# Optimization experiments

Measured on AMD Instinct MI355X. Metric: run time of the kernel, lower is better.

## Reference

```python
import jax, jax.numpy as jnp
import numpy as np

VOCAB = 50257
FEAT = 512
EPS = 1e-12  # F.normalize default eps


def setup_inputs() -> dict:
    key = jax.random.key(0)
    k1, k2, k3 = jax.random.split(key, 3)
    token_ids = jax.random.randint(k1, (32, 4096), 0, VOCAB)
    # nn.Linear(vocab, feat): weight [FEAT, VOCAB], bias [FEAT]
    W = jax.random.normal(k2, (FEAT, VOCAB), dtype=jnp.float32) * 0.02
    b = jax.random.normal(k3, (FEAT,), dtype=jnp.float32) * 0.02
    return {"token_ids": token_ids, "W": W, "b": b}


def reference(token_ids, W, b):
    # one_hot(ids) @ W.T + b  ==  gather rows of W.T at ids, then add bias
    feats = W.T[token_ids] + b  # [B, S, FEAT]
    norm = jnp.sqrt(jnp.sum(feats * feats, axis=-1, keepdims=True))
    return feats / jnp.maximum(norm, EPS)
```

## Files before the change

### kernel.cpp

```cpp
#include <hip/hip_runtime.h>
#include <hip/hip_bf16.h>

#define VOCAB 50257
#define FEAT 512
#define NTOK (32 * 4096)
#define EPS 1e-12f
#define NFT 8

typedef float f32x4 __attribute__((ext_vector_type(4)));

__device__ __forceinline__ unsigned short f2bf(float x) {
    __hip_bfloat16 h = __float2bfloat16(x);
    unsigned short u;
    __builtin_memcpy(&u, &h, 2);
    return u;
}
__device__ __forceinline__ float bfround(float x) {
    return __bfloat162float(__float2bfloat16(x));
}
__device__ __forceinline__ float bflo(unsigned int w) {
    unsigned int u = w << 16; float f; __builtin_memcpy(&f, &u, 4); return f;
}
__device__ __forceinline__ float bfhi(unsigned int w) {
    unsigned int u = w & 0xffff0000u; float f; __builtin_memcpy(&f, &u, 4); return f;
}

__global__ __launch_bounds__(256) void transpose_bias_bf16(
        const float* __restrict__ W, const float* __restrict__ b,
        unsigned short* __restrict__ Wt, float* __restrict__ partial) {
    __shared__ float tile[64][65];
    __shared__ float psum[4][64];
    const int t  = threadIdx.x;
    const int l  = t & 63;
    const int w  = t >> 6;
    const int v0 = blockIdx.x * 64;
    const int f0 = blockIdx.y * 64;
    const int c  = l & 15;
    const int r  = l >> 4;
    const int vb = v0 + c * 4;

    float p[4] = {0.f, 0.f, 0.f, 0.f};
#pragma unroll
    for (int k = 0; k < 4; ++k) {
        const int fl = w * 16 + k * 4 + r;
        const int f  = f0 + fl;
        f32x4 x;
        if (vb + 3 < VOCAB) {
            __builtin_memcpy(&x, W + (size_t)f * VOCAB + vb, 16);
        } else {
#pragma unroll
            for (int i = 0; i < 4; ++i)
                x[i] = (vb + i < VOCAB) ? W[(size_t)f * VOCAB + vb + i] : 0.0f;
        }
        const float bf = b[f];
#pragma unroll
        for (int i = 0; i < 4; ++i) {
            const float xi = x[i] + bf;
            tile[fl][c * 4 + i] = xi;
            const float xr = bfround(xi);
            p[i] += xr * xr;
        }
    }

#pragma unroll
    for (int i = 0; i < 4; ++i) {
        float s = p[i];
        s += __shfl_xor(s, 16, 64);
        s += __shfl_xor(s, 32, 64);
        if (r == 0) psum[w][c * 4 + i] = s;
    }
    __syncthreads();

    if (t < 64) {
        const int v = v0 + t;
        if (v < VOCAB)
            partial[blockIdx.y * VOCAB + v] =
                psum[0][t] + psum[1][t] + psum[2][t] + psum[3][t];
    }

#pragma unroll
    for (int ps = 0; ps < 2; ++ps) {
        const int idx = t + 256 * ps;
        const int vl  = idx >> 3;
        const int ch  = idx & 7;
        const int v   = v0 + vl;
        if (v < VOCAB) {
            unsigned int pk[4];
#pragma unroll
            for (int j = 0; j < 4; ++j) {
                const int f = ch * 8 + 2 * j;
                pk[j] = (unsigned int)f2bf(tile[f][vl]) |
                        ((unsigned int)f2bf(tile[f + 1][vl]) << 16);
            }
            *(uint4*)(Wt + (size_t)v * FEAT + f0 + ch * 8) =
                make_uint4(pk[0], pk[1], pk[2], pk[3]);
        }
    }
}

__global__ __launch_bounds__(256) void norm_table(const float* __restrict__ partial,
                                                  float* __restrict__ invn) {
    const int v = blockIdx.x * 256 + threadIdx.x;
    if (v >= VOCAB) return;
    float s = 0.0f;
#pragma unroll
    for (int j = 0; j < NFT; ++j) s += partial[j * VOCAB + v];
    invn[v] = 1.0f / fmaxf(sqrtf(s), EPS);
}

__global__ __launch_bounds__(256) void encode_bf16(
        const int* __restrict__ ids, const unsigned short* __restrict__ Wt,
        const float* __restrict__ invn, float* __restrict__ out) {
    const int tok  = (int)((blockIdx.x * (unsigned long long)blockDim.x + threadIdx.x) >> 6);
    const int lane = threadIdx.x & 63;
    if (tok >= NTOK) return;

    const int id = ids[tok];
    const uint4 rr = *(const uint4*)(Wt + (size_t)id * FEAT + lane * 8);
    const float inv = invn[id];

    float x[8];
    x[0] = bflo(rr.x); x[1] = bfhi(rr.x);
    x[2] = bflo(rr.y); x[3] = bfhi(rr.y);
    x[4] = bflo(rr.z); x[5] = bfhi(rr.z);
    x[6] = bflo(rr.w); x[7] = bfhi(rr.w);

    f32x4 o0 = {x[0] * inv, x[1] * inv, x[2] * inv, x[3] * inv};
    f32x4 o1 = {x[4] * inv, x[5] * inv, x[6] * inv, x[7] * inv};
    f32x4* dst = (f32x4*)(out + (size_t)tok * FEAT + lane * 8);
    __builtin_nontemporal_store(o0, dst);
    __builtin_nontemporal_store(o1, dst + 1);
}

__global__ __launch_bounds__(256) void encode_direct(const int* __restrict__ ids,
                                                     const float* __restrict__ W,
                                                     const float* __restrict__ bias,
                                                     float* __restrict__ out) {
    const int tok  = (int)((blockIdx.x * (unsigned long long)blockDim.x + threadIdx.x) >> 6);
    const int lane = threadIdx.x & 63;
    if (tok >= NTOK) return;

    const int id = ids[tok];
    float x[8];
    float s = 0.0f;
#pragma unroll
    for (int j = 0; j < 8; ++j) {
        const int f = lane * 8 + j;
        x[j] = W[(size_t)f * VOCAB + id] + bias[f];
        s += x[j] * x[j];
    }
#pragma unroll
    for (int off = 32; off > 0; off >>= 1)
        s += __shfl_xor(s, off, 64);

    const float inv = 1.0f / fmaxf(sqrtf(s), EPS);
    float4 o0 = make_float4(x[0] * inv, x[1] * inv, x[2] * inv, x[3] * inv);
    float4 o1 = make_float4(x[4] * inv, x[5] * inv, x[6] * inv, x[7] * inv);
    float4* dst = (float4*)(out + (size_t)tok * FEAT + lane * 8);
    dst[0] = o0;
    dst[1] = o1;
}

extern "C" void kernel_launch(void* const* d_in, const int* in_sizes, int n_in,
                              void* d_out, int out_size, void* d_ws, size_t ws_size,
                              hipStream_t stream) {
    const int*   ids  = (const int*)d_in[0];
    const float* W    = (const float*)d_in[1];
    const float* bias = (const float*)d_in[2];
    float*       out  = (float*)d_out;

    const size_t wt_bytes   = (size_t)VOCAB * FEAT * sizeof(unsigned short);
    const size_t part_bytes = (size_t)NFT * VOCAB * sizeof(float);
    const size_t inv_bytes  = (size_t)VOCAB * sizeof(float);
    const int nblocks = NTOK / 4;

    if (ws_size >= wt_bytes + part_bytes + inv_bytes) {
        unsigned short* Wt = (unsigned short*)d_ws;
        float* partial     = (float*)((char*)d_ws + wt_bytes);
        float* invn        = (float*)((char*)d_ws + wt_bytes + part_bytes);
        dim3 tgrid((VOCAB + 63) / 64, FEAT / 64);
        transpose_bias_bf16<<<tgrid, 256, 0, stream>>>(W, bias, Wt, partial);
        norm_table<<<(VOCAB + 255) / 256, 256, 0, stream>>>(partial, invn);
        encode_bf16<<<nblocks, 256, 0, stream>>>(ids, Wt, invn, out);
    } else {
        encode_direct<<<nblocks, 256, 0, stream>>>(ids, W, bias, out);
    }
}
```

Baseline: 134.7 us.

## Fuse transpose, norm table and gather into one cooperative persistent kernel

Replaces the three-kernel pipeline (transpose+bias to bf16, norm table, gather-normalize) with a single cooperative kernel of 512 blocks x 512 threads that uses grid.sync between phases. The gather phase becomes persistent, with each wave looping over tokens and software-prefetching the next row. The intent is to remove launch gaps and tail effects between kernels. In exchange it adds two grid-wide barriers and limits occupancy to a fixed grid, and it falls back to the old path if the cooperative launch fails.

```diff
diff --git a/kernel.cpp b/kernel.cpp
--- a/kernel.cpp
+++ b/kernel.cpp
@@ -1,19 +1,28 @@
 #include <hip/hip_runtime.h>
 #include <hip/hip_bf16.h>
+#include <hip/hip_cooperative_groups.h>
+
+namespace cg = cooperative_groups;
 
 #define VOCAB 50257
 #define FEAT 512
 #define NTOK (32 * 4096)
 #define EPS 1e-12f
 #define NFT 8
+#define NVT 786
+#define NTILES (NVT * NFT)
+#define NBLK 512
+#define NTHR 512
+#define NSG (NBLK * 2)
+#define P1_ITERS ((NTILES + NSG - 1) / NSG)
+#define NWAVE (NBLK * (NTHR / 64))
+#define P2_ITERS (NTOK / NWAVE)
 
 typedef float f32x4 __attribute__((ext_vector_type(4)));
 
 __device__ __forceinline__ unsigned short f2bf(float x) {
     __hip_bfloat16 h = __float2bfloat16(x);
-    unsigned short u;
-    __builtin_memcpy(&u, &h, 2);
-    return u;
+    unsigned short u; __builtin_memcpy(&u, &h, 2); return u;
 }
 __device__ __forceinline__ float bfround(float x) {
     return __bfloat162float(__float2bfloat16(x));
@@ -23,6 +32,140 @@
 }
 __device__ __forceinline__ float bfhi(unsigned int w) {
     unsigned int u = w & 0xffff0000u; float f; __builtin_memcpy(&f, &u, 4); return f;
+}
+
+__global__ __launch_bounds__(NTHR, 4) void fused_encoder(
+        const int* __restrict__ ids, const float* __restrict__ W,
+        const float* __restrict__ b, unsigned short* __restrict__ Wt,
+        float* __restrict__ partial, float* __restrict__ invn,
+        float* __restrict__ out) {
+    cg::grid_group grid = cg::this_grid();
+
+    __shared__ float tile[2][64][65];
+    __shared__ float psum[2][4][64];
+
+    const int t   = threadIdx.x;
+    const int sg  = t >> 8;
+    const int st  = t & 255;
+    const int l   = st & 63;
+    const int w   = st >> 6;
+    const int c   = l & 15;
+    const int r   = l >> 4;
+    const int gsg = blockIdx.x * 2 + sg;
+
+    for (int i = 0; i < P1_ITERS; ++i) {
+        const int tileIdx = gsg + i * NSG;
+        const bool active = tileIdx < NTILES;
+        const int vt = active ? (tileIdx >> 3) : 0;
+        const int ft = active ? (tileIdx & 7) : 0;
+        const int v0 = vt * 64, f0 = ft * 64;
+        const int vb = v0 + c * 4;
+
+        float p[4] = {0.f, 0.f, 0.f, 0.f};
+        if (active) {
+#pragma unroll
+            for (int k = 0; k < 4; ++k) {
+                const int fl = w * 16 + k * 4 + r;
+                const int f  = f0 + fl;
+                f32x4 x;
+                if (vb + 3 < VOCAB) {
+                    __builtin_memcpy(&x, W + (size_t)f * VOCAB + vb, 16);
+                } else {
+#pragma unroll
+                    for (int q = 0; q < 4; ++q)
+                        x[q] = (vb + q < VOCAB) ? W[(size_t)f * VOCAB + vb + q] : 0.0f;
+                }
+                const float bf = b[f];
+#pragma unroll
+                for (int q = 0; q < 4; ++q) {
+                    const float xi = x[q] + bf;
+                    tile[sg][fl][c * 4 + q] = xi;
+                    const float xr = bfround(xi);
+                    p[q] += xr * xr;
+                }
+            }
+        }
+#pragma unroll
+        for (int q = 0; q < 4; ++q) {
+            float s = p[q];
+            s += __shfl_xor(s, 16, 64);
+            s += __shfl_xor(s, 32, 64);
+            if (r == 0) psum[sg][w][c * 4 + q] = s;
+        }
+        __syncthreads();
+
+        if (active && st < 64) {
+            const int v = v0 + st;
+            if (v < VOCAB)
+                partial[ft * VOCAB + v] =
+                    psum[sg][0][st] + psum[sg][1][st] + psum[sg][2][st] + psum[sg][3][st];
+        }
+        if (active) {
+#pragma unroll
+            for (int ps = 0; ps < 2; ++ps) {
+                const int idx = st + 256 * ps;
+                const int vl  = idx >> 3;
+                const int ch  = idx & 7;
+                const int v   = v0 + vl;
+                if (v < VOCAB) {
+                    unsigned int pk[4];
+#pragma unroll
+                    for (int j = 0; j < 4; ++j) {
+                        const int f = ch * 8 + 2 * j;
+                        pk[j] = (unsigned int)f2bf(tile[sg][f][vl]) |
+                                ((unsigned int)f2bf(tile[sg][f + 1][vl]) << 16);
+                    }
+                    *(uint4*)(Wt + (size_t)v * FEAT + f0 + ch * 8) =
+                        make_uint4(pk[0], pk[1], pk[2], pk[3]);
+                }
+            }
+        }
+        __syncthreads();
+    }
+
+    grid.sync();
+
+    {
+        const int v = blockIdx.x * NTHR + t;
+        if (v < VOCAB) {
+            float s = 0.0f;
+#pragma unroll
+            for (int j = 0; j < NFT; ++j) s += partial[j * VOCAB + v];
+            invn[v] = 1.0f / fmaxf(sqrtf(s), EPS);
+        }
+    }
+
+    grid.sync();
+
+    {
+        const int gw = blockIdx.x * (NTHR / 64) + (t >> 6);
+
+        int   id = ids[gw];
+        uint4 rr = *((const uint4*)(Wt + (size_t)id * FEAT) + l);
+        float iv = invn[id];
+
+#pragma unroll 1
+        for (int it = 0; it < P2_ITERS; ++it) {
+            const bool more = it + 1 < P2_ITERS;
+            const int   idn = more ? ids[(it + 1) * NWAVE + gw] : 0;
+            const uint4 rn  = *((const uint4*)(Wt + (size_t)idn * FEAT) + l);
+            const float ivn = invn[idn];
+
+            float x[8];
+            x[0] = bflo(rr.x); x[1] = bfhi(rr.x);
+            x[2] = bflo(rr.y); x[3] = bfhi(rr.y);
+            x[4] = bflo(rr.z); x[5] = bfhi(rr.z);
+            x[6] = bflo(rr.w); x[7] = bfhi(rr.w);
+
+            f32x4 o0 = {x[0] * iv, x[1] * iv, x[2] * iv, x[3] * iv};
+            f32x4 o1 = {x[4] * iv, x[5] * iv, x[6] * iv, x[7] * iv};
+            f32x4* dst = (f32x4*)(out + (size_t)(it * NWAVE + gw) * FEAT + l * 8);
+            __builtin_nontemporal_store(o0, dst);
+            __builtin_nontemporal_store(o1, dst + 1);
+
+            rr = rn; iv = ivn;
+        }
+    }
 }
 
 __global__ __launch_bounds__(256) void transpose_bias_bf16(
@@ -30,13 +173,9 @@
         unsigned short* __restrict__ Wt, float* __restrict__ partial) {
     __shared__ float tile[64][65];
     __shared__ float psum[4][64];
-    const int t  = threadIdx.x;
-    const int l  = t & 63;
-    const int w  = t >> 6;
-    const int v0 = blockIdx.x * 64;
-    const int f0 = blockIdx.y * 64;
-    const int c  = l & 15;
-    const int r  = l >> 4;
+    const int t = threadIdx.x, l = t & 63, w = t >> 6;
+    const int v0 = blockIdx.x * 64, f0 = blockIdx.y * 64;
+    const int c = l & 15, r = l >> 4;
     const int vb = v0 + c * 4;
 
     float p[4] = {0.f, 0.f, 0.f, 0.f};
@@ -49,41 +188,37 @@
             __builtin_memcpy(&x, W + (size_t)f * VOCAB + vb, 16);
         } else {
 #pragma unroll
-            for (int i = 0; i < 4; ++i)
-                x[i] = (vb + i < VOCAB) ? W[(size_t)f * VOCAB + vb + i] : 0.0f;
+            for (int q = 0; q < 4; ++q)
+                x[q] = (vb + q < VOCAB) ? W[(size_t)f * VOCAB + vb + q] : 0.0f;
         }
         const float bf = b[f];
 #pragma unroll
-        for (int i = 0; i < 4; ++i) {
-            const float xi = x[i] + bf;
-            tile[fl][c * 4 + i] = xi;
+        for (int q = 0; q < 4; ++q) {
+            const float xi = x[q] + bf;
+            tile[fl][c * 4 + q] = xi;
             const float xr = bfround(xi);
-            p[i] += xr * xr;
-        }
-    }
-
-#pragma unroll
-    for (int i = 0; i < 4; ++i) {
-        float s = p[i];
+            p[q] += xr * xr;
+        }
+    }
+#pragma unroll
+    for (int q = 0; q < 4; ++q) {
+        float s = p[q];
         s += __shfl_xor(s, 16, 64);
         s += __shfl_xor(s, 32, 64);
-        if (r == 0) psum[w][c * 4 + i] = s;
+        if (r == 0) psum[w][c * 4 + q] = s;
     }
     __syncthreads();
-
     if (t < 64) {
         const int v = v0 + t;
         if (v < VOCAB)
             partial[blockIdx.y * VOCAB + v] =
                 psum[0][t] + psum[1][t] + psum[2][t] + psum[3][t];
     }
-
 #pragma unroll
     for (int ps = 0; ps < 2; ++ps) {
         const int idx = t + 256 * ps;
-        const int vl  = idx >> 3;
-        const int ch  = idx & 7;
-        const int v   = v0 + vl;
+        const int vl = idx >> 3, ch = idx & 7;
+        const int v = v0 + vl;
         if (v < VOCAB) {
             unsigned int pk[4];
 #pragma unroll
@@ -114,17 +249,14 @@
     const int tok  = (int)((blockIdx.x * (unsigned long long)blockDim.x + threadIdx.x) >> 6);
     const int lane = threadIdx.x & 63;
     if (tok >= NTOK) return;
-
     const int id = ids[tok];
-    const uint4 rr = *(const uint4*)(Wt + (size_t)id * FEAT + lane * 8);
+    const uint4 rr = *((const uint4*)(Wt + (size_t)id * FEAT) + lane);
     const float inv = invn[id];
-
     float x[8];
     x[0] = bflo(rr.x); x[1] = bfhi(rr.x);
     x[2] = bflo(rr.y); x[3] = bfhi(rr.y);
     x[4] = bflo(rr.z); x[5] = bfhi(rr.z);
     x[6] = bflo(rr.w); x[7] = bfhi(rr.w);
-
     f32x4 o0 = {x[0] * inv, x[1] * inv, x[2] * inv, x[3] * inv};
     f32x4 o1 = {x[4] * inv, x[5] * inv, x[6] * inv, x[7] * inv};
     f32x4* dst = (f32x4*)(out + (size_t)tok * FEAT + lane * 8);
@@ -139,7 +271,6 @@
     const int tok  = (int)((blockIdx.x * (unsigned long long)blockDim.x + threadIdx.x) >> 6);
     const int lane = threadIdx.x & 63;
     if (tok >= NTOK) return;
-
     const int id = ids[tok];
     float x[8];
     float s = 0.0f;
@@ -152,7 +283,6 @@
 #pragma unroll
     for (int off = 32; off > 0; off >>= 1)
         s += __shfl_xor(s, off, 64);
-
     const float inv = 1.0f / fmaxf(sqrtf(s), EPS);
     float4 o0 = make_float4(x[0] * inv, x[1] * inv, x[2] * inv, x[3] * inv);
     float4 o1 = make_float4(x[4] * inv, x[5] * inv, x[6] * inv, x[7] * inv);
@@ -172,17 +302,23 @@
     const size_t wt_bytes   = (size_t)VOCAB * FEAT * sizeof(unsigned short);
     const size_t part_bytes = (size_t)NFT * VOCAB * sizeof(float);
     const size_t inv_bytes  = (size_t)VOCAB * sizeof(float);
-    const int nblocks = NTOK / 4;
 
     if (ws_size >= wt_bytes + part_bytes + inv_bytes) {
         unsigned short* Wt = (unsigned short*)d_ws;
         float* partial     = (float*)((char*)d_ws + wt_bytes);
         float* invn        = (float*)((char*)d_ws + wt_bytes + part_bytes);
-        dim3 tgrid((VOCAB + 63) / 64, FEAT / 64);
-        transpose_bias_bf16<<<tgrid, 256, 0, stream>>>(W, bias, Wt, partial);
-        norm_table<<<(VOCAB + 255) / 256, 256, 0, stream>>>(partial, invn);
-        encode_bf16<<<nblocks, 256, 0, stream>>>(ids, Wt, invn, out);
+
+        void* args[] = {(void*)&ids, (void*)&W, (void*)&bias,
+                        (void*)&Wt, (void*)&partial, (void*)&invn, (void*)&out};
+        hipError_t err = hipLaunchCooperativeKernel(
+            (const void*)fused_encoder, dim3(NBLK), dim3(NTHR), args, 0, stream);
+        if (err != hipSuccess) {
+            dim3 tgrid((VOCAB + 63) / 64, FEAT / 64);
+            transpose_bias_bf16<<<tgrid, 256, 0, stream>>>(W, bias, Wt, partial);
+            norm_table<<<(VOCAB + 255) / 256, 256, 0, stream>>>(partial, invn);
+            encode_bf16<<<NTOK / 4, 256, 0, stream>>>(ids, Wt, invn, out);
+        }
     } else {
-        encode_direct<<<nblocks, 256, 0, stream>>>(ids, W, bias, out);
-    }
-}
+        encode_direct<<<NTOK / 4, 256, 0, stream>>>(ids, W, bias, out);
+    }
+}
```

Measured after the change: 245.4 us. 82.1% more time.
